# Kernel tuning notes

Measured on AMD Instinct MI355X. Metric: run time of the kernel, lower is better.

## Reference

```python
import jax, jax.numpy as jnp
import numpy as np

NEG_SLOPE = 0.2

def gat_layer(x, src, dst, W, a_src, a_dst, b, n_nodes):
    # x: [N, Fin]; src/dst: [E] (self-loops already appended)
    h = x @ W                                   # [N, Fout]
    s = h @ a_src                               # [N] per-node source attention term
    d = h @ a_dst                               # [N]
    e = jax.nn.leaky_relu(s[src] + d[dst], NEG_SLOPE)   # [E]
    # softmax over incoming edges of each dst node (numerically stable)
    m = jax.ops.segment_max(e, dst, num_segments=n_nodes)
    m = jnp.where(jnp.isfinite(m), m, 0.0)
    ex = jnp.exp(e - m[dst])
    z = jax.ops.segment_sum(ex, dst, num_segments=n_nodes)
    alpha = ex / z[dst]                         # [E]
    out = jax.ops.segment_sum(alpha[:, None] * h[src], dst, num_segments=n_nodes)
    return out + b

def setup_inputs() -> dict:
    key = jax.random.key(0)
    ks = jax.random.split(key, 12)
    N, E, F_IN, F_OUT = 50000, 800000, 128, 128
    H = 2 * F_OUT  # 256, conv1 output width
    x = jax.random.normal(ks[0], (N, F_IN), dtype=jnp.float32)
    edge_index = jax.random.randint(ks[1], (2, E), 0, N, dtype=jnp.int64)
    glorot = lambda k, shape: jax.random.uniform(k, shape, jnp.float32, -1.0, 1.0) * jnp.sqrt(6.0 / sum(shape))
    return {
        "x": x,
        "edge_index": edge_index,
        "W1": glorot(ks[2], (F_IN, H)),
        "a_src1": glorot(ks[3], (H,)) * 0.1,
        "a_dst1": glorot(ks[4], (H,)) * 0.1,
        "b1": jnp.zeros((H,), jnp.float32),
        "W2": glorot(ks[5], (H, F_OUT)),
        "a_src2": glorot(ks[6], (F_OUT,)) * 0.1,
        "a_dst2": glorot(ks[7], (F_OUT,)) * 0.1,
        "b2": jnp.zeros((F_OUT,), jnp.float32),
    }

def reference(x, edge_index, W1, a_src1, a_dst1, b1, W2, a_src2, a_dst2, b2):
    n_nodes = x.shape[0]
    # PyG GATConv adds self-loops by default
    loops = jnp.arange(n_nodes, dtype=edge_index.dtype)
    src = jnp.concatenate([edge_index[0], loops])
    dst = jnp.concatenate([edge_index[1], loops])
    h = gat_layer(x, src, dst, W1, a_src1, a_dst1, b1, n_nodes)
    h = jax.nn.relu(h)
    return gat_layer(h, src, dst, W2, a_src2, a_dst2, b2, n_nodes)
```

## Files before the change

kernel.cpp:

```cpp
#include <hip/hip_runtime.h>
#include <hip/hip_bf16.h>


#define NEG_SLOPE 0.2f
#define NB 416
#define EPB 2048
#define NBUCKET 1568
#define BSH 5

typedef __attribute__((ext_vector_type(8))) short bf16x8;
typedef __attribute__((ext_vector_type(4))) float f32x4;

__device__ __forceinline__ unsigned short f2bf(float v) {
    __hip_bfloat16 b = __float2bfloat16(v);
    return *reinterpret_cast<unsigned short*>(&b);
}
__device__ __forceinline__ float bf2f(unsigned short u) {
    __hip_bfloat16 b = *reinterpret_cast<__hip_bfloat16*>(&u);
    return __bfloat162float(b);
}

__global__ __launch_bounds__(256) void hist_wprep_k(
    const int* __restrict__ dstE, const float* __restrict__ W1,
    const float* __restrict__ W2, const float* __restrict__ a_src1,
    const float* __restrict__ a_dst1, int* __restrict__ histG,
    unsigned short* __restrict__ w1T, unsigned short* __restrict__ w2T,
    float* __restrict__ w_s1, float* __restrict__ w_d1, int E, int N) {
    const int b = blockIdx.x;
    if (b < NB) {
        __shared__ int h[NBUCKET];
        for (int i = threadIdx.x; i < NBUCKET; i += 256) h[i] = 0;
        __syncthreads();
        const int base = b * EPB;
        const int total = E + N;
        #pragma unroll
        for (int q = 0; q < EPB / 256; ++q) {
            int i = base + q * 256 + threadIdx.x;
            if (i < total) {
                int di = (i < E) ? dstE[i] : i - E;
                atomicAdd(&h[di >> BSH], 1);
            }
        }
        __syncthreads();
        for (int i = threadIdx.x; i < NBUCKET; i += 256)
            histG[b * NBUCKET + i] = h[i];
    } else if (b < NB + 128) {
        int i = (b - NB) * 256 + threadIdx.x;
        int k = i >> 8, n = i & 255;
        w1T[n * 128 + k] = f2bf(W1[i]);
    } else if (b < NB + 256) {
        int j = (b - NB - 128) * 256 + threadIdx.x;
        int k = j >> 7, n = j & 127;
        w2T[n * 256 + k] = f2bf(W2[j]);
    } else {
        int w = ((b - NB - 256) * 256 + threadIdx.x) >> 6;
        int lane = threadIdx.x & 63;
        const float* row = W1 + (size_t)w * 256;
        float ss = 0.f, dd = 0.f;
        #pragma unroll
        for (int f = lane; f < 256; f += 64) {
            float v = row[f];
            ss += v * a_src1[f];
            dd += v * a_dst1[f];
        }
        #pragma unroll
        for (int off = 32; off; off >>= 1) {
            ss += __shfl_down(ss, off);
            dd += __shfl_down(dd, off);
        }
        if (lane == 0) { w_s1[w] = ss; w_d1[w] = dd; }
    }
}

__global__ __launch_bounds__(256) void colscan_xprep_k(
    int* __restrict__ histG, int* __restrict__ colSum,
    const float* __restrict__ x, const float* __restrict__ va,
    const float* __restrict__ vb, unsigned short* __restrict__ xbf,
    float* __restrict__ s, float* __restrict__ d, int N) {
    const int b = blockIdx.x;
    constexpr int CSB = NBUCKET / 4;
    if (b < CSB) {
        const int bkt = b * 4 + (threadIdx.x >> 6);
        const int l = threadIdx.x & 63;
        int carry = 0;
        #pragma unroll
        for (int c = 0; c < (NB + 63) / 64; ++c) {
            int blk = c * 64 + l;
            int v = (blk < NB) ? histG[blk * NBUCKET + bkt] : 0;
            int incl = v;
            #pragma unroll
            for (int off = 1; off < 64; off <<= 1) {
                int t = __shfl_up(incl, off);
                if (l >= off) incl += t;
            }
            if (blk < NB) histG[blk * NBUCKET + bkt] = carry + (incl - v);
            carry += __shfl(incl, 63);
        }
        if (l == 0) colSum[bkt] = carry;
    } else {
        int w = (((b - CSB) * 256) + threadIdx.x) >> 6;
        int lane = threadIdx.x & 63;
        if (w >= N) return;
        float2 v = *(const float2*)(x + (size_t)w * 128 + lane * 2);
        ushort2 u;
        u.x = f2bf(v.x);
        u.y = f2bf(v.y);
        *(ushort2*)(xbf + (size_t)w * 128 + lane * 2) = u;
        float ss = v.x * va[lane * 2] + v.y * va[lane * 2 + 1];
        float dd = v.x * vb[lane * 2] + v.y * vb[lane * 2 + 1];
        #pragma unroll
        for (int off = 32; off; off >>= 1) {
            ss += __shfl_down(ss, off);
            dd += __shfl_down(dd, off);
        }
        if (lane == 0) { s[w] = ss; d[w] = dd; }
    }
}

__global__ __launch_bounds__(256) void bscatter_k(
    const int* __restrict__ srcE, const int* __restrict__ dstE,
    const int* __restrict__ histG, const int* __restrict__ colSum,
    unsigned* __restrict__ packed, int E, int N) {
    __shared__ int bb_s[NBUCKET];
    __shared__ int cur[NBUCKET];
    __shared__ int wsum[4];
    const int tid = threadIdx.x;
    {
        const int lane = tid & 63, wv = tid >> 6;
        const int base = tid * 7;
        int loc[7];
        int ssum = 0;
        #pragma unroll
        for (int q = 0; q < 7; ++q) {
            int idx = base + q;
            int c = (idx < NBUCKET) ? colSum[idx] : 0;
            loc[q] = ssum;
            ssum += c;
        }
        int incl = ssum;
        #pragma unroll
        for (int off = 1; off < 64; off <<= 1) {
            int t = __shfl_up(incl, off);
            if (lane >= off) incl += t;
        }
        if (lane == 63) wsum[wv] = incl;
        __syncthreads();
        if (tid == 0) {
            int r = 0;
            #pragma unroll
            for (int i = 0; i < 4; ++i) { int c = wsum[i]; wsum[i] = r; r += c; }
        }
        __syncthreads();
        const int b0 = wsum[wv] + (incl - ssum);
        #pragma unroll
        for (int q = 0; q < 7; ++q) {
            int idx = base + q;
            if (idx < NBUCKET) bb_s[idx] = b0 + loc[q];
        }
    }
    for (int i = tid; i < NBUCKET; i += 256) cur[i] = 0;
    __syncthreads();
    const int b = blockIdx.x;
    const int base = b * EPB;
    const int total = E + N;
    #pragma unroll
    for (int q = 0; q < EPB / 256; ++q) {
        int i = base + q * 256 + tid;
        if (i < total) {
            int di, si;
            if (i < E) { di = dstE[i]; si = srcE[i]; }
            else       { di = si = i - E; }
            int bk = di >> BSH;
            int r = atomicAdd(&cur[bk], 1);
            packed[bb_s[bk] + histG[b * NBUCKET + bk] + r] =
                ((unsigned)di << 16) | (unsigned)si;
        }
    }
}

__global__ __launch_bounds__(256) void bsort_k(
    const unsigned* __restrict__ packed, const int* __restrict__ colSum,
    int* __restrict__ ssrc, int* __restrict__ rowptr, int EA, int N) {
    __shared__ unsigned arr[2048];
    __shared__ int cnt[32], pf[32], cur[32];
    __shared__ int red[4];
    __shared__ int beg_s;
    const int b = blockIdx.x;
    const int tid = threadIdx.x;
    {
        int part = 0;
        for (int i = tid; i < b; i += 256) part += colSum[i];
        #pragma unroll
        for (int off = 32; off; off >>= 1) part += __shfl_down(part, off);
        if ((tid & 63) == 0) red[tid >> 6] = part;
        __syncthreads();
        if (tid == 0) beg_s = red[0] + red[1] + red[2] + red[3];
    }
    if (tid < 32) cnt[tid] = 0;
    __syncthreads();
    const int beg = beg_s;
    const int L = colSum[b];
    for (int t = tid; t < L; t += 256) {
        unsigned e = packed[beg + t];
        arr[t] = e;
        atomicAdd(&cnt[(e >> 16) & 31], 1);
    }
    __syncthreads();
    if (tid == 0) {
        int r = 0;
        #pragma unroll
        for (int j = 0; j < 32; ++j) { pf[j] = r; cur[j] = r; r += cnt[j]; }
    }
    __syncthreads();
    if (tid < 32) {
        int dd = b * 32 + tid;
        if (dd < N) rowptr[dd] = beg + pf[tid];
    }
    for (int t = tid; t < L; t += 256) {
        unsigned e = arr[t];
        int r = atomicAdd(&cur[(e >> 16) & 31], 1);
        ssrc[beg + r] = (int)(e & 0xffffu);
    }
    if (b == 0 && tid == 0) rowptr[N] = EA;
}

template <int K, int NN, int EPI>
__global__ __launch_bounds__(256) void gemm_bf16(
    const unsigned short* __restrict__ A, const unsigned short* __restrict__ BT,
    unsigned short* __restrict__ C, const float* __restrict__ bias,
    const float* __restrict__ va, const float* __restrict__ vb,
    float* __restrict__ sOut, float* __restrict__ dOut, int M) {
    constexpr int BK = 32, PAD = 8;
    __shared__ short As[128][BK + PAD];
    __shared__ short Bs[128][BK + PAD];
    const int tid = threadIdx.x;
    const int wv = tid >> 6;
    const int ln = tid & 63;
    const int row0 = blockIdx.x * 128;
    const int col0 = blockIdx.y * 128;

    f32x4 acc[2][8];
    #pragma unroll
    for (int m = 0; m < 2; ++m)
        #pragma unroll
        for (int n = 0; n < 8; ++n) acc[m][n] = {0.f, 0.f, 0.f, 0.f};

    const int l15 = ln & 15;
    const int kg = (ln >> 4) * 8;

    for (int k0 = 0; k0 < K; k0 += BK) {
        #pragma unroll
        for (int t = 0; t < 2; ++t) {
            int v = tid + t * 256;
            int r = v >> 2;
            int kc = (v & 3) * 8;
            bf16x8 val = {0, 0, 0, 0, 0, 0, 0, 0};
            int gr = row0 + r;
            if (gr < M)
                val = *(const bf16x8*)(A + (size_t)gr * K + k0 + kc);
            *(bf16x8*)(&As[r][kc]) = val;
        }
        #pragma unroll
        for (int t = 0; t < 2; ++t) {
            int v = tid + t * 256;
            int c = v >> 2;
            int kc = (v & 3) * 8;
            *(bf16x8*)(&Bs[c][kc]) =
                *(const bf16x8*)(BT + (size_t)(col0 + c) * K + k0 + kc);
        }
        __syncthreads();

        bf16x8 ah[2], bh[8];
        #pragma unroll
        for (int m = 0; m < 2; ++m)
            ah[m] = *(const bf16x8*)&As[wv * 32 + m * 16 + l15][kg];
        #pragma unroll
        for (int n = 0; n < 8; ++n)
            bh[n] = *(const bf16x8*)&Bs[n * 16 + l15][kg];
        #pragma unroll
        for (int m = 0; m < 2; ++m)
            #pragma unroll
            for (int n = 0; n < 8; ++n)
                acc[m][n] = __builtin_amdgcn_mfma_f32_16x16x32_bf16(
                    ah[m], bh[n], acc[m][n], 0, 0, 0);
        __syncthreads();
    }

    const int crow = (ln >> 4) * 4;
    #pragma unroll
    for (int m = 0; m < 2; ++m) {
        #pragma unroll
        for (int q = 0; q < 4; ++q) {
            int gr = row0 + wv * 32 + m * 16 + crow + q;
            if (gr >= M) continue;
            if constexpr (EPI == 1) {
                #pragma unroll
                for (int n = 0; n < 8; ++n) {
                    int gc = col0 + n * 16 + l15;
                    float v = acc[m][n][q] + bias[gc];
                    v = fmaxf(v, 0.f);
                    C[(size_t)gr * NN + gc] = f2bf(v);
                }
            } else {
                float sp = 0.f, dp = 0.f;
                #pragma unroll
                for (int n = 0; n < 8; ++n) {
                    int gc = n * 16 + l15;
                    float v = acc[m][n][q];
                    C[(size_t)gr * NN + gc] = f2bf(v);
                    sp += v * va[gc];
                    dp += v * vb[gc];
                }
                #pragma unroll
                for (int off = 1; off < 16; off <<= 1) {
                    sp += __shfl_xor(sp, off);
                    dp += __shfl_xor(dp, off);
                }
                if (l15 == 0) { sOut[gr] = sp; dOut[gr] = dp; }
            }
        }
    }
}

template <bool OUTBF>
__global__ __launch_bounds__(256) void node_gather_k(
    const int* __restrict__ rowptr, const int* __restrict__ ssrc,
    const float* __restrict__ s, const float* __restrict__ d,
    const unsigned short* __restrict__ hsrc, const float* __restrict__ bias,
    unsigned short* __restrict__ obf, float* __restrict__ outf, int N) {
    constexpr int F = 128, G = 8;
    const int node = blockIdx.x * 4 + (threadIdx.x >> 6);
    const int lane = threadIdx.x & 63;
    if (node >= N) return;
    const int beg = rowptr[node];
    const int end = rowptr[node + 1];
    const float dn = d[node];
    const int grp = lane >> 3;
    const int lr = lane & 7;

    float acc[16] = {};
    float zsum = 0.f;
    int j = beg + grp;
    for (; j + G < end; j += 2 * G) {
        int sj0 = ssrc[j];
        int sj1 = ssrc[j + G];
        float e0 = s[sj0] + dn;
        float e1 = s[sj1] + dn;
        const unsigned short* r0 = hsrc + (size_t)sj0 * F + lr * 16;
        const unsigned short* r1 = hsrc + (size_t)sj1 * F + lr * 16;
        bf16x8 v0a = *(const bf16x8*)r0;
        bf16x8 v0b = *(const bf16x8*)(r0 + 8);
        bf16x8 v1a = *(const bf16x8*)r1;
        bf16x8 v1b = *(const bf16x8*)(r1 + 8);
        e0 = (e0 > 0.f) ? e0 : NEG_SLOPE * e0;
        e1 = (e1 > 0.f) ? e1 : NEG_SLOPE * e1;
        float x0 = __expf(e0);
        float x1 = __expf(e1);
        zsum += x0 + x1;
        #pragma unroll
        for (int q = 0; q < 8; ++q) {
            acc[q]     += x0 * bf2f(((unsigned short*)&v0a)[q]);
            acc[q + 8] += x0 * bf2f(((unsigned short*)&v0b)[q]);
            acc[q]     += x1 * bf2f(((unsigned short*)&v1a)[q]);
            acc[q + 8] += x1 * bf2f(((unsigned short*)&v1b)[q]);
        }
    }
    if (j < end) {
        int sj = ssrc[j];
        float e = s[sj] + dn;
        e = (e > 0.f) ? e : NEG_SLOPE * e;
        float exj = __expf(e);
        zsum += exj;
        const unsigned short* r0 = hsrc + (size_t)sj * F + lr * 16;
        bf16x8 va_ = *(const bf16x8*)r0;
        bf16x8 vb_ = *(const bf16x8*)(r0 + 8);
        #pragma unroll
        for (int q = 0; q < 8; ++q) {
            acc[q]     += exj * bf2f(((unsigned short*)&va_)[q]);
            acc[q + 8] += exj * bf2f(((unsigned short*)&vb_)[q]);
        }
    }
    #pragma unroll
    for (int off = 8; off < 64; off <<= 1) {
        zsum += __shfl_xor(zsum, off);
        #pragma unroll
        for (int q = 0; q < 16; ++q) acc[q] += __shfl_xor(acc[q], off);
    }
    const float inv = 1.f / zsum;

    if (lane < 8) {
        if constexpr (OUTBF) {
            bf16x8 w0, w1;
            #pragma unroll
            for (int q = 0; q < 8; ++q) {
                ((unsigned short*)&w0)[q] = f2bf(acc[q] * inv);
                ((unsigned short*)&w1)[q] = f2bf(acc[q + 8] * inv);
            }
            *(bf16x8*)(obf + (size_t)node * F + lr * 16) = w0;
            *(bf16x8*)(obf + (size_t)node * F + lr * 16 + 8) = w1;
        } else {
            float o[16];
            #pragma unroll
            for (int q = 0; q < 16; ++q)
                o[q] = acc[q] * inv + bias[lr * 16 + q];
            float* op = outf + (size_t)node * F + lr * 16;
            *(float4*)op = {o[0], o[1], o[2], o[3]};
            *(float4*)(op + 4) = {o[4], o[5], o[6], o[7]};
            *(float4*)(op + 8) = {o[8], o[9], o[10], o[11]};
            *(float4*)(op + 12) = {o[12], o[13], o[14], o[15]};
        }
    }
}

extern "C" void kernel_launch(void* const* d_in, const int* in_sizes, int n_in,
                              void* d_out, int out_size, void* d_ws, size_t ws_size,
                              hipStream_t stream) {
    const float* x      = (const float*)d_in[0];
    const int*   eidx   = (const int*)d_in[1];
    const float* W1     = (const float*)d_in[2];
    const float* a_src1 = (const float*)d_in[3];
    const float* a_dst1 = (const float*)d_in[4];
    const float* b1     = (const float*)d_in[5];
    const float* W2     = (const float*)d_in[6];
    const float* a_src2 = (const float*)d_in[7];
    const float* a_dst2 = (const float*)d_in[8];
    const float* b2     = (const float*)d_in[9];

    const int N = in_sizes[0] / 128;
    const int E = in_sizes[1] / 2;
    const int F_IN = 128, H = 256, F_OUT = 128;
    const int EA = E + N;

    const int* srcE = eidx;
    const int* dstE = eidx + E;

    unsigned short* xbf    = (unsigned short*)d_ws;
    unsigned short* aggx   = xbf + (size_t)N * F_IN;
    unsigned short* g1     = aggx + (size_t)N * F_IN;
    unsigned short* h2bf   = g1 + (size_t)N * H;
    float*          sbuf   = (float*)(h2bf + (size_t)N * F_OUT);
    float*          dbuf   = sbuf + N;
    float*          w_s1   = dbuf + N;
    float*          w_d1   = w_s1 + F_IN;
    unsigned short* w1T    = (unsigned short*)(w_d1 + F_IN);
    unsigned short* w2T    = w1T + 32768;
    int*            rowptr = (int*)(w2T + 32768);
    int*            histG  = rowptr + (N + 1);
    int*            colSum = histG + NB * NBUCKET;
    int*            ssrc   = colSum + NBUCKET;
    unsigned*       packed = (unsigned*)(ssrc + EA);

    float* out = (float*)d_out;
    const int xblocks = (N * 64 + 255) / 256;

    hist_wprep_k<<<NB + 288, 256, 0, stream>>>(
        dstE, W1, W2, a_src1, a_dst1, histG, w1T, w2T, w_s1, w_d1, E, N);
    colscan_xprep_k<<<NBUCKET / 4 + xblocks, 256, 0, stream>>>(
        histG, colSum, x, w_s1, w_d1, xbf, sbuf, dbuf, N);
    bscatter_k<<<NB, 256, 0, stream>>>(srcE, dstE, histG, colSum, packed, E, N);
    bsort_k<<<NBUCKET, 256, 0, stream>>>(packed, colSum, ssrc, rowptr, EA, N);

    {
        int nb = (N + 3) / 4;
        node_gather_k<true><<<nb, 256, 0, stream>>>(
            rowptr, ssrc, sbuf, dbuf, xbf, nullptr, aggx, nullptr, N);
    }
    {
        dim3 gg((N + 127) / 128, H / 128);
        gemm_bf16<128, 256, 1><<<gg, 256, 0, stream>>>(
            aggx, w1T, g1, b1, nullptr, nullptr, nullptr, nullptr, N);
    }
    {
        dim3 gg((N + 127) / 128, 1);
        gemm_bf16<256, 128, 2><<<gg, 256, 0, stream>>>(
            g1, w2T, h2bf, nullptr, a_src2, a_dst2, sbuf, dbuf, N);
    }
    {
        int nb = (N + 3) / 4;
        node_gather_k<false><<<nb, 256, 0, stream>>>(
            rowptr, ssrc, sbuf, dbuf, h2bf, b2, nullptr, out, N);
    }
}
```

Baseline: 145.4 us.

## Fuse bucket sort with layer-1 neighbor aggregation into one kernel

```diff
diff --git a/kernel.cpp b/kernel.cpp
--- a/kernel.cpp
+++ b/kernel.cpp
@@ -178,10 +178,14 @@
     }
 }
 
-__global__ __launch_bounds__(256) void bsort_k(
+__global__ __launch_bounds__(256) void bsort_gather1_k(
     const unsigned* __restrict__ packed, const int* __restrict__ colSum,
-    int* __restrict__ ssrc, int* __restrict__ rowptr, int EA, int N) {
+    int* __restrict__ ssrc, int* __restrict__ rowptr,
+    const float* __restrict__ s, const float* __restrict__ d,
+    const unsigned short* __restrict__ xbf, unsigned short* __restrict__ aggx,
+    int EA, int N) {
     __shared__ unsigned arr[2048];
+    __shared__ unsigned short sorted[2048];
     __shared__ int cnt[32], pf[32], cur[32];
     __shared__ int red[4];
     __shared__ int beg_s;
@@ -219,9 +223,84 @@
     for (int t = tid; t < L; t += 256) {
         unsigned e = arr[t];
         int r = atomicAdd(&cur[(e >> 16) & 31], 1);
-        ssrc[beg + r] = (int)(e & 0xffffu);
+        int src = (int)(e & 0xffffu);
+        sorted[r] = (unsigned short)src;
+        ssrc[beg + r] = src;
     }
     if (b == 0 && tid == 0) rowptr[N] = EA;
+    __syncthreads();
+
+    constexpr int F = 128, G = 8;
+    const int wv = tid >> 6;
+    const int lane = tid & 63;
+    const int grp = lane >> 3;
+    const int lr = lane & 7;
+    for (int nd = wv * 8; nd < wv * 8 + 8; ++nd) {
+        const int dd = b * 32 + nd;
+        if (dd >= N) continue;
+        const int lbeg = pf[nd];
+        const int lend = pf[nd] + cnt[nd];
+        const float dn = d[dd];
+        float acc[16] = {};
+        float zsum = 0.f;
+        int j = lbeg + grp;
+        for (; j + G < lend; j += 2 * G) {
+            int sj0 = sorted[j];
+            int sj1 = sorted[j + G];
+            float e0 = s[sj0] + dn;
+            float e1 = s[sj1] + dn;
+            const unsigned short* r0 = xbf + (size_t)sj0 * F + lr * 16;
+            const unsigned short* r1 = xbf + (size_t)sj1 * F + lr * 16;
+            bf16x8 v0a = *(const bf16x8*)r0;
+            bf16x8 v0b = *(const bf16x8*)(r0 + 8);
+            bf16x8 v1a = *(const bf16x8*)r1;
+            bf16x8 v1b = *(const bf16x8*)(r1 + 8);
+            e0 = (e0 > 0.f) ? e0 : NEG_SLOPE * e0;
+            e1 = (e1 > 0.f) ? e1 : NEG_SLOPE * e1;
+            float x0 = __expf(e0);
+            float x1 = __expf(e1);
+            zsum += x0 + x1;
+            #pragma unroll
+            for (int q = 0; q < 8; ++q) {
+                acc[q]     += x0 * bf2f(((unsigned short*)&v0a)[q]);
+                acc[q + 8] += x0 * bf2f(((unsigned short*)&v0b)[q]);
+                acc[q]     += x1 * bf2f(((unsigned short*)&v1a)[q]);
+                acc[q + 8] += x1 * bf2f(((unsigned short*)&v1b)[q]);
+            }
+        }
+        if (j < lend) {
+            int sj = sorted[j];
+            float e = s[sj] + dn;
+            e = (e > 0.f) ? e : NEG_SLOPE * e;
+            float exj = __expf(e);
+            zsum += exj;
+            const unsigned short* r0 = xbf + (size_t)sj * F + lr * 16;
+            bf16x8 va_ = *(const bf16x8*)r0;
+            bf16x8 vb_ = *(const bf16x8*)(r0 + 8);
+            #pragma unroll
+            for (int q = 0; q < 8; ++q) {
+                acc[q]     += exj * bf2f(((unsigned short*)&va_)[q]);
+                acc[q + 8] += exj * bf2f(((unsigned short*)&vb_)[q]);
+            }
+        }
+        #pragma unroll
+        for (int off = 8; off < 64; off <<= 1) {
+            zsum += __shfl_xor(zsum, off);
+            #pragma unroll
+            for (int q = 0; q < 16; ++q) acc[q] += __shfl_xor(acc[q], off);
+        }
+        const float inv = 1.f / zsum;
+        if (lane < 8) {
+            bf16x8 w0, w1;
+            #pragma unroll
+            for (int q = 0; q < 8; ++q) {
+                ((unsigned short*)&w0)[q] = f2bf(acc[q] * inv);
+                ((unsigned short*)&w1)[q] = f2bf(acc[q + 8] * inv);
+            }
+            *(bf16x8*)(aggx + (size_t)dd * F + lr * 16) = w0;
+            *(bf16x8*)(aggx + (size_t)dd * F + lr * 16 + 8) = w1;
+        }
+    }
 }
 
 template <int K, int NN, int EPI>
@@ -322,12 +401,11 @@
     }
 }
 
-template <bool OUTBF>
-__global__ __launch_bounds__(256) void node_gather_k(
+__global__ __launch_bounds__(256) void node_gather2_k(
     const int* __restrict__ rowptr, const int* __restrict__ ssrc,
     const float* __restrict__ s, const float* __restrict__ d,
     const unsigned short* __restrict__ hsrc, const float* __restrict__ bias,
-    unsigned short* __restrict__ obf, float* __restrict__ outf, int N) {
+    float* __restrict__ outf, int N) {
     constexpr int F = 128, G = 8;
     const int node = blockIdx.x * 4 + (threadIdx.x >> 6);
     const int lane = threadIdx.x & 63;
@@ -389,26 +467,15 @@
     const float inv = 1.f / zsum;
 
     if (lane < 8) {
-        if constexpr (OUTBF) {
-            bf16x8 w0, w1;
-            #pragma unroll
-            for (int q = 0; q < 8; ++q) {
-                ((unsigned short*)&w0)[q] = f2bf(acc[q] * inv);
-                ((unsigned short*)&w1)[q] = f2bf(acc[q + 8] * inv);
-            }
-            *(bf16x8*)(obf + (size_t)node * F + lr * 16) = w0;
-            *(bf16x8*)(obf + (size_t)node * F + lr * 16 + 8) = w1;
-        } else {
-            float o[16];
-            #pragma unroll
-            for (int q = 0; q < 16; ++q)
-                o[q] = acc[q] * inv + bias[lr * 16 + q];
-            float* op = outf + (size_t)node * F + lr * 16;
-            *(float4*)op = {o[0], o[1], o[2], o[3]};
-            *(float4*)(op + 4) = {o[4], o[5], o[6], o[7]};
-            *(float4*)(op + 8) = {o[8], o[9], o[10], o[11]};
-            *(float4*)(op + 12) = {o[12], o[13], o[14], o[15]};
-        }
+        float o[16];
+        #pragma unroll
+        for (int q = 0; q < 16; ++q)
+            o[q] = acc[q] * inv + bias[lr * 16 + q];
+        float* op = outf + (size_t)node * F + lr * 16;
+        *(float4*)op = {o[0], o[1], o[2], o[3]};
+        *(float4*)(op + 4) = {o[4], o[5], o[6], o[7]};
+        *(float4*)(op + 8) = {o[8], o[9], o[10], o[11]};
+        *(float4*)(op + 12) = {o[12], o[13], o[14], o[15]};
     }
 }
 
@@ -458,13 +525,8 @@
     colscan_xprep_k<<<NBUCKET / 4 + xblocks, 256, 0, stream>>>(
         histG, colSum, x, w_s1, w_d1, xbf, sbuf, dbuf, N);
     bscatter_k<<<NB, 256, 0, stream>>>(srcE, dstE, histG, colSum, packed, E, N);
-    bsort_k<<<NBUCKET, 256, 0, stream>>>(packed, colSum, ssrc, rowptr, EA, N);
-
-    {
-        int nb = (N + 3) / 4;
-        node_gather_k<true><<<nb, 256, 0, stream>>>(
-            rowptr, ssrc, sbuf, dbuf, xbf, nullptr, aggx, nullptr, N);
-    }
+    bsort_gather1_k<<<NBUCKET, 256, 0, stream>>>(
+        packed, colSum, ssrc, rowptr, sbuf, dbuf, xbf, aggx, EA, N);
     {
         dim3 gg((N + 127) / 128, H / 128);
         gemm_bf16<128, 256, 1><<<gg, 256, 0, stream>>>(
@@ -477,7 +539,7 @@
     }
     {
         int nb = (N + 3) / 4;
-        node_gather_k<false><<<nb, 256, 0, stream>>>(
-            rowptr, ssrc, sbuf, dbuf, h2bf, b2, nullptr, out, N);
-    }
-}
+        node_gather2_k<<<nb, 256, 0, stream>>>(
+            rowptr, ssrc, sbuf, dbuf, h2bf, b2, out, N);
+    }
+}
```

Result: slower. 151.0 us (+3.9%).
